# Kernel optimization log

Hardware: AMD Instinct MI355X
Metric: run time of the kernel (lower is better)

The kernel has to match this reference:

```python
import jax, jax.numpy as jnp
import numpy as np

B, C, V = 1024, 512, 256  # batch, num_conjunctions, num_variables


def setup_inputs() -> dict:
    key = jax.random.key(0)
    k1, k2, k3 = jax.random.split(key, 3)
    x0 = jax.random.uniform(k1, (B, V), dtype=jnp.float32)
    # torch init: conj = 1 - 2*rand  -> uniform in (-1, 1)
    conjunctions = 1.0 - 2.0 * jax.random.uniform(k2, (C, 2 * V), dtype=jnp.float32)
    # rw = 10 - 20*rand -> uniform in (-10, 10)
    rule_weights = 10.0 - 20.0 * jax.random.uniform(k3, (C,), dtype=jnp.float32)
    return {"x0": x0, "conjunctions": conjunctions, "rule_weights": rule_weights}


def reference(x0, conjunctions, rule_weights):
    mu = jax.nn.sigmoid(conjunctions)            # (C, 2V)
    x = jnp.concatenate((x0, 1.0 - x0), axis=1)  # (B, 2V)
    # fuzzy-AND: broadcast mul-add then min over literal axis
    x_pot = mu[None, :, :] * x[:, None, :] + (1.0 - mu)[None, :, :]  # (B, C, 2V)
    fit = jnp.min(x_pot, axis=-1)                # (B, C)
    return 5.0 + jnp.sum(rule_weights * fit, axis=-1)  # (B,)
```

## Files before the change

### kernel.cpp

```cpp
#include <hip/hip_runtime.h>


#define B_    1024
#define C_    512
#define V_    256
#define TWOV  512

#define CPW    64
#define NCHUNK (C_ / CPW)
#define BPB    16
#define NBG    (B_ / BPB)
#define WAVES  8
#define VPW    32
#define HVP    8

__global__ __launch_bounds__(256) void k_prep(const float* __restrict__ conj,
                                              float2* __restrict__ muT2,
                                              float* __restrict__ out) {
    const int c = blockIdx.x;
    const int v = threadIdx.x;
    if (c < 4) out[c * 256 + v] = 5.0f;
    float z1 = conj[(size_t)c * TWOV + v];
    float z2 = conj[(size_t)c * TWOV + V_ + v];
    float m1 = 1.0f / (1.0f + __expf(-z1));
    float m2 = 1.0f / (1.0f + __expf(-z2));
    muT2[(size_t)(v >> 1) * (2 * C_) + c * 2 + (v & 1)] = make_float2(m1, m2);
}

__global__ __launch_bounds__(512, 4) void k_main(const float* __restrict__ x0,
                                                 const float4* __restrict__ muT4,
                                                 const float* __restrict__ rw,
                                                 float* __restrict__ out) {
    const int tid   = threadIdx.x;
    const int lane  = tid & 63;
    const int wave  = tid >> 6;
    const int chunk = blockIdx.y;
    const int c     = chunk * CPW + lane;
    const int bg    = blockIdx.x;
    const int v0    = wave * VPW;

    __shared__ float4 xs[BPB * V_ / 4];
    __shared__ float  red[BPB * WAVES * 64];

    {
        const float4* xg = reinterpret_cast<const float4*>(x0 + (size_t)bg * BPB * V_);
        xs[tid]       = xg[tid];
        xs[tid + 512] = xg[tid + 512];
    }

    const float4* mup = muT4 + (size_t)(v0 >> 1) * C_ + c;

    float m[BPB];
#pragma unroll
    for (int i = 0; i < BPB; ++i) m[i] = 0.0f;

    __syncthreads();

#pragma unroll
    for (int h = 0; h < 2; ++h) {
        float4 mr[HVP];
#pragma unroll
        for (int p = 0; p < HVP; ++p)
            mr[p] = mup[(size_t)(h * HVP + p) * C_];
#pragma unroll
        for (int p = 0; p < HVP; ++p)
            asm volatile("" : "+v"(mr[p].x), "+v"(mr[p].y), "+v"(mr[p].z), "+v"(mr[p].w));

#pragma unroll
        for (int bi = 0; bi < BPB; ++bi) {
            const int xb = bi * (V_ / 4) + (v0 >> 2) + h * 4;
            float4 xa = xs[xb + 0];
            float4 xc = xs[xb + 1];
            float4 xd = xs[xb + 2];
            float4 xe = xs[xb + 3];
            float mm = m[bi];
#define STEP(P, XA, XB) \
            mm = fmaxf(mm, fmaxf(__builtin_fmaf(-mr[P].x, (XA), mr[P].x), mr[P].y * (XA))); \
            mm = fmaxf(mm, fmaxf(__builtin_fmaf(-mr[P].z, (XB), mr[P].z), mr[P].w * (XB)));
            STEP(0, xa.x, xa.y)  STEP(1, xa.z, xa.w)
            STEP(2, xc.x, xc.y)  STEP(3, xc.z, xc.w)
            STEP(4, xd.x, xd.y)  STEP(5, xd.z, xd.w)
            STEP(6, xe.x, xe.y)  STEP(7, xe.z, xe.w)
#undef STEP
            m[bi] = mm;
        }
    }

#pragma unroll
    for (int bi = 0; bi < BPB; ++bi)
        red[bi * (WAVES * 64) + tid] = m[bi];
    __syncthreads();

    const float rwc = rw[c];
    float m0 = red[wave * (WAVES * 64) + lane];
    float m1 = red[(wave + 8) * (WAVES * 64) + lane];
#pragma unroll
    for (int k = 1; k < WAVES; ++k) {
        m0 = fmaxf(m0, red[wave * (WAVES * 64) + k * 64 + lane]);
        m1 = fmaxf(m1, red[(wave + 8) * (WAVES * 64) + k * 64 + lane]);
    }
    float s0 = rwc * (1.0f - m0);
    float s1 = rwc * (1.0f - m1);
#pragma unroll
    for (int d = 1; d < 64; d <<= 1) {
        s0 += __shfl_xor(s0, d, 64);
        s1 += __shfl_xor(s1, d, 64);
    }
    if (lane == 0) {
        atomicAdd(&out[bg * BPB + wave], s0);
        atomicAdd(&out[bg * BPB + wave + 8], s1);
    }
}

__global__ __launch_bounds__(256) void k_naive(const float* __restrict__ x0,
                                               const float* __restrict__ conj,
                                               const float* __restrict__ rw,
                                               float* __restrict__ out) {
    int b = blockIdx.x;
    int t = threadIdx.x;
    __shared__ float red[256];
    float acc = 0.0f;
    for (int c = t; c < C_; c += 256) {
        float m = 0.0f;
        for (int v = 0; v < V_; ++v) {
            float mu1 = 1.0f / (1.0f + expf(-conj[(size_t)c * TWOV + v]));
            float mu2 = 1.0f / (1.0f + expf(-conj[(size_t)c * TWOV + V_ + v]));
            float x = x0[(size_t)b * V_ + v];
            m = fmaxf(m, fmaxf(mu1 * (1.0f - x), mu2 * x));
        }
        acc += rw[c] * (1.0f - m);
    }
    red[t] = acc;
    __syncthreads();
    for (int s = 128; s > 0; s >>= 1) {
        if (t < s) red[t] += red[t + s];
        __syncthreads();
    }
    if (t == 0) out[b] = 5.0f + red[0];
}

extern "C" void kernel_launch(void* const* d_in, const int* in_sizes, int n_in,
                              void* d_out, int out_size, void* d_ws, size_t ws_size,
                              hipStream_t stream) {
    const float* x0   = (const float*)d_in[0];
    const float* conj = (const float*)d_in[1];
    const float* rw   = (const float*)d_in[2];
    float* out = (float*)d_out;

    const size_t mu_floats = (size_t)(V_ / 2) * C_ * 4;
    const size_t need = mu_floats * sizeof(float);

    if (ws_size < need) {
        k_naive<<<B_, 256, 0, stream>>>(x0, conj, rw, out);
        return;
    }

    float4* muT4 = (float4*)d_ws;

    k_prep<<<C_, 256, 0, stream>>>(conj, (float2*)muT4, out);
    dim3 grid(NBG, NCHUNK);
    k_main<<<grid, 512, 0, stream>>>(x0, muT4, rw, out);
}
```

Before: 24.89 us.

## Restructure main kernel tiling with register double-buffered global loads instead of LDS

```diff
diff --git a/kernel.cpp b/kernel.cpp
--- a/kernel.cpp
+++ b/kernel.cpp
@@ -6,13 +6,10 @@
 #define V_    256
 #define TWOV  512
 
-#define CPW    64
-#define NCHUNK (C_ / CPW)
-#define BPB    16
+#define BPB    8
 #define NBG    (B_ / BPB)
+#define NCH    4
 #define WAVES  8
-#define VPW    32
-#define HVP    8
 
 __global__ __launch_bounds__(256) void k_prep(const float* __restrict__ conj,
                                               float2* __restrict__ muT2,
@@ -31,84 +28,129 @@
                                                  const float4* __restrict__ muT4,
                                                  const float* __restrict__ rw,
                                                  float* __restrict__ out) {
-    const int tid   = threadIdx.x;
-    const int lane  = tid & 63;
-    const int wave  = tid >> 6;
-    const int chunk = blockIdx.y;
-    const int c     = chunk * CPW + lane;
-    const int bg    = blockIdx.x;
-    const int v0    = wave * VPW;
-
-    __shared__ float4 xs[BPB * V_ / 4];
-    __shared__ float  red[BPB * WAVES * 64];
-
-    {
-        const float4* xg = reinterpret_cast<const float4*>(x0 + (size_t)bg * BPB * V_);
-        xs[tid]       = xg[tid];
-        xs[tid + 512] = xg[tid + 512];
-    }
-
-    const float4* mup = muT4 + (size_t)(v0 >> 1) * C_ + c;
+    const int tid    = threadIdx.x;
+    const int lane   = tid & 63;
+    const int wave_u = __builtin_amdgcn_readfirstlane(tid >> 6);
+    const int t      = wave_u & 1;
+    const int s      = wave_u >> 1;
+    const int bg     = blockIdx.x;
+    const int chunk  = blockIdx.y;
+    const int c      = chunk * 128 + t * 64 + lane;
+    const int v0     = s * 64;
+
+    const float* xb = x0 + (size_t)bg * BPB * V_ + v0;
+
+    const float4* mu1p = muT4 + (size_t)(v0 >> 1) * C_ + c;
+    const float4* mu2p = mu1p + C_;
+
+    const float rwc = rw[c];
 
     float m[BPB];
 #pragma unroll
     for (int i = 0; i < BPB; ++i) m[i] = 0.0f;
 
-    __syncthreads();
-
-#pragma unroll
-    for (int h = 0; h < 2; ++h) {
-        float4 mr[HVP];
-#pragma unroll
-        for (int p = 0; p < HVP; ++p)
-            mr[p] = mup[(size_t)(h * HVP + p) * C_];
-#pragma unroll
-        for (int p = 0; p < HVP; ++p)
-            asm volatile("" : "+v"(mr[p].x), "+v"(mr[p].y), "+v"(mr[p].z), "+v"(mr[p].w));
-
-#pragma unroll
-        for (int bi = 0; bi < BPB; ++bi) {
-            const int xb = bi * (V_ / 4) + (v0 >> 2) + h * 4;
-            float4 xa = xs[xb + 0];
-            float4 xc = xs[xb + 1];
-            float4 xd = xs[xb + 2];
-            float4 xe = xs[xb + 3];
-            float mm = m[bi];
-#define STEP(P, XA, XB) \
-            mm = fmaxf(mm, fmaxf(__builtin_fmaf(-mr[P].x, (XA), mr[P].x), mr[P].y * (XA))); \
-            mm = fmaxf(mm, fmaxf(__builtin_fmaf(-mr[P].z, (XB), mr[P].z), mr[P].w * (XB)));
-            STEP(0, xa.x, xa.y)  STEP(1, xa.z, xa.w)
-            STEP(2, xc.x, xc.y)  STEP(3, xc.z, xc.w)
-            STEP(4, xd.x, xd.y)  STEP(5, xd.z, xd.w)
-            STEP(6, xe.x, xe.y)  STEP(7, xe.z, xe.w)
-#undef STEP
-            m[bi] = mm;
-        }
-    }
-
+    float4 XA0, XA1, XA2, XA3, XA4, XA5, XA6, XA7;
+    float4 XB0, XB1, XB2, XB3, XB4, XB5, XB6, XB7;
+    float4 ma0, mb0, ma1, mb1;
+
+#define XL(X, q) do { \
+    X##0 = *reinterpret_cast<const float4*>(xb + 0 * V_ + 4 * (q)); \
+    X##1 = *reinterpret_cast<const float4*>(xb + 1 * V_ + 4 * (q)); \
+    X##2 = *reinterpret_cast<const float4*>(xb + 2 * V_ + 4 * (q)); \
+    X##3 = *reinterpret_cast<const float4*>(xb + 3 * V_ + 4 * (q)); \
+    X##4 = *reinterpret_cast<const float4*>(xb + 4 * V_ + 4 * (q)); \
+    X##5 = *reinterpret_cast<const float4*>(xb + 5 * V_ + 4 * (q)); \
+    X##6 = *reinterpret_cast<const float4*>(xb + 6 * V_ + 4 * (q)); \
+    X##7 = *reinterpret_cast<const float4*>(xb + 7 * V_ + 4 * (q)); \
+} while (0)
+
+#define MUL_NEXT(MA, MB) do { \
+    MA = mu1p[0]; MB = mu2p[0]; mu1p += 2 * C_; mu2p += 2 * C_; \
+} while (0)
+
+#define PINM(MA, MB) \
+    asm volatile("" : "+v"(MA.x), "+v"(MA.y), "+v"(MA.z), "+v"(MA.w), \
+                      "+v"(MB.x), "+v"(MB.y), "+v"(MB.z), "+v"(MB.w))
+
+#define CB(XV, MA, MB, bi) do { \
+    float mm = m[bi]; \
+    mm = fmaxf(fmaxf(__builtin_fmaf(-(MA).x, (XV).x, (MA).x), (MA).y * (XV).x), mm); \
+    mm = fmaxf(fmaxf(__builtin_fmaf(-(MA).z, (XV).y, (MA).z), (MA).w * (XV).y), mm); \
+    mm = fmaxf(fmaxf(__builtin_fmaf(-(MB).x, (XV).z, (MB).x), (MB).y * (XV).z), mm); \
+    mm = fmaxf(fmaxf(__builtin_fmaf(-(MB).z, (XV).w, (MB).z), (MB).w * (XV).w), mm); \
+    m[bi] = mm; } while (0)
+
+#define COMPUTE(X, MA, MB) do { \
+    CB(X##0, MA, MB, 0); CB(X##1, MA, MB, 1); \
+    CB(X##2, MA, MB, 2); CB(X##3, MA, MB, 3); \
+    CB(X##4, MA, MB, 4); CB(X##5, MA, MB, 5); \
+    CB(X##6, MA, MB, 6); CB(X##7, MA, MB, 7); } while (0)
+
+    XL(XA, 0);
+    MUL_NEXT(ma0, mb0);
+
+#define QSTEP(q, XC, XN, MAC, MBC, MAN, MBN) do { \
+    XL(XN, (q) + 1);               \
+    MUL_NEXT(MAN, MBN);            \
+    PINM(MAC, MBC);                \
+    COMPUTE(XC, MAC, MBC); } while (0)
+
+    QSTEP( 0, XA, XB, ma0, mb0, ma1, mb1);
+    QSTEP( 1, XB, XA, ma1, mb1, ma0, mb0);
+    QSTEP( 2, XA, XB, ma0, mb0, ma1, mb1);
+    QSTEP( 3, XB, XA, ma1, mb1, ma0, mb0);
+    QSTEP( 4, XA, XB, ma0, mb0, ma1, mb1);
+    QSTEP( 5, XB, XA, ma1, mb1, ma0, mb0);
+    QSTEP( 6, XA, XB, ma0, mb0, ma1, mb1);
+    QSTEP( 7, XB, XA, ma1, mb1, ma0, mb0);
+    QSTEP( 8, XA, XB, ma0, mb0, ma1, mb1);
+    QSTEP( 9, XB, XA, ma1, mb1, ma0, mb0);
+    QSTEP(10, XA, XB, ma0, mb0, ma1, mb1);
+    QSTEP(11, XB, XA, ma1, mb1, ma0, mb0);
+    QSTEP(12, XA, XB, ma0, mb0, ma1, mb1);
+    QSTEP(13, XB, XA, ma1, mb1, ma0, mb0);
+    QSTEP(14, XA, XB, ma0, mb0, ma1, mb1);
+    PINM(ma1, mb1);
+    COMPUTE(XB, ma1, mb1);
+
+#undef QSTEP
+#undef COMPUTE
+#undef CB
+#undef PINM
+#undef MUL_NEXT
+#undef XL
+
+    __shared__ float red[4 * 128 * 9];
+    const int ci = t * 64 + lane;
 #pragma unroll
     for (int bi = 0; bi < BPB; ++bi)
-        red[bi * (WAVES * 64) + tid] = m[bi];
+        red[(s * 128 + ci) * 9 + bi] = m[bi];
     __syncthreads();
 
-    const float rwc = rw[c];
-    float m0 = red[wave * (WAVES * 64) + lane];
-    float m1 = red[(wave + 8) * (WAVES * 64) + lane];
-#pragma unroll
-    for (int k = 1; k < WAVES; ++k) {
-        m0 = fmaxf(m0, red[wave * (WAVES * 64) + k * 64 + lane]);
-        m1 = fmaxf(m1, red[(wave + 8) * (WAVES * 64) + k * 64 + lane]);
-    }
-    float s0 = rwc * (1.0f - m0);
-    float s1 = rwc * (1.0f - m1);
-#pragma unroll
-    for (int d = 1; d < 64; d <<= 1) {
-        s0 += __shfl_xor(s0, d, 64);
-        s1 += __shfl_xor(s1, d, 64);
-    }
-    if (lane == 0) {
-        atomicAdd(&out[bg * BPB + wave], s0);
-        atomicAdd(&out[bg * BPB + wave + 8], s1);
+    if (wave_u < 2) {
+        float con0, con1, con2, con3, con4, con5, con6, con7;
+#define FIN(bi, CON) do { \
+        float mm = red[(0 * 128 + ci) * 9 + bi]; \
+        mm = fmaxf(mm, red[(1 * 128 + ci) * 9 + bi]); \
+        mm = fmaxf(mm, red[(2 * 128 + ci) * 9 + bi]); \
+        mm = fmaxf(mm, red[(3 * 128 + ci) * 9 + bi]); \
+        float v = rwc * (1.0f - mm); \
+        v += __shfl_xor(v, 1, 64);  v += __shfl_xor(v, 2, 64); \
+        v += __shfl_xor(v, 4, 64);  v += __shfl_xor(v, 8, 64); \
+        v += __shfl_xor(v, 16, 64); v += __shfl_xor(v, 32, 64); \
+        CON = v; } while (0)
+        FIN(0, con0); FIN(1, con1); FIN(2, con2); FIN(3, con3);
+        FIN(4, con4); FIN(5, con5); FIN(6, con6); FIN(7, con7);
+#undef FIN
+        float t0 = (lane & 1) ? con1 : con0;
+        float t1 = (lane & 1) ? con3 : con2;
+        float t2 = (lane & 1) ? con5 : con4;
+        float t3 = (lane & 1) ? con7 : con6;
+        float u0 = (lane & 2) ? t1 : t0;
+        float u1 = (lane & 2) ? t3 : t2;
+        float sel = (lane & 4) ? u1 : u0;
+        if (lane < 8)
+            atomicAdd(&out[bg * BPB + lane], sel);
     }
 }
 
@@ -158,6 +200,6 @@
     float4* muT4 = (float4*)d_ws;
 
     k_prep<<<C_, 256, 0, stream>>>(conj, (float2*)muT4, out);
-    dim3 grid(NBG, NCHUNK);
+    dim3 grid(NBG, NCH);
     k_main<<<grid, 512, 0, stream>>>(x0, muT4, rw, out);
 }
```

Result: faster. 22.02 us (-11.5%).

## Retile main kernel into 8x4 register blocks with LDS-staged x and mu

Applied to the files above, without the earlier changes.

```diff
diff --git a/kernel.cpp b/kernel.cpp
--- a/kernel.cpp
+++ b/kernel.cpp
@@ -4,111 +4,157 @@
 #define B_    1024
 #define C_    512
 #define V_    256
-#define TWOV  512
-
-#define CPW    64
-#define NCHUNK (C_ / CPW)
-#define BPB    16
-#define NBG    (B_ / BPB)
-#define WAVES  8
-#define VPW    32
-#define HVP    8
+
+#define BT    64
+#define CT    32
+#define VC    128
 
 __global__ __launch_bounds__(256) void k_prep(const float* __restrict__ conj,
-                                              float2* __restrict__ muT2,
+                                              float* __restrict__ muP,
                                               float* __restrict__ out) {
     const int c = blockIdx.x;
     const int v = threadIdx.x;
     if (c < 4) out[c * 256 + v] = 5.0f;
-    float z1 = conj[(size_t)c * TWOV + v];
-    float z2 = conj[(size_t)c * TWOV + V_ + v];
+    float z1 = conj[(size_t)c * 512 + v];
+    float z2 = conj[(size_t)c * 512 + 256 + v];
     float m1 = 1.0f / (1.0f + __expf(-z1));
     float m2 = 1.0f / (1.0f + __expf(-z2));
-    muT2[(size_t)(v >> 1) * (2 * C_) + c * 2 + (v & 1)] = make_float2(m1, m2);
-}
-
-__global__ __launch_bounds__(512, 4) void k_main(const float* __restrict__ x0,
-                                                 const float4* __restrict__ muT4,
+    size_t base = (size_t)v * 1024 + (size_t)(c >> 2) * 8 + (c & 3);
+    muP[base]     = m1;
+    muP[base + 4] = m2;
+}
+
+__global__ __launch_bounds__(512, 2) void k_main(const float* __restrict__ x0,
+                                                 const float* __restrict__ muP,
                                                  const float* __restrict__ rw,
                                                  float* __restrict__ out) {
-    const int tid   = threadIdx.x;
-    const int lane  = tid & 63;
-    const int wave  = tid >> 6;
-    const int chunk = blockIdx.y;
-    const int c     = chunk * CPW + lane;
-    const int bg    = blockIdx.x;
-    const int v0    = wave * VPW;
-
-    __shared__ float4 xs[BPB * V_ / 4];
-    __shared__ float  red[BPB * WAVES * 64];
-
-    {
-        const float4* xg = reinterpret_cast<const float4*>(x0 + (size_t)bg * BPB * V_);
-        xs[tid]       = xg[tid];
-        xs[tid + 512] = xg[tid + 512];
-    }
-
-    const float4* mup = muT4 + (size_t)(v0 >> 1) * C_ + c;
-
-    float m[BPB];
-#pragma unroll
-    for (int i = 0; i < BPB; ++i) m[i] = 0.0f;
-
-    __syncthreads();
-
-#pragma unroll
-    for (int h = 0; h < 2; ++h) {
-        float4 mr[HVP];
-#pragma unroll
-        for (int p = 0; p < HVP; ++p)
-            mr[p] = mup[(size_t)(h * HVP + p) * C_];
-#pragma unroll
-        for (int p = 0; p < HVP; ++p)
-            asm volatile("" : "+v"(mr[p].x), "+v"(mr[p].y), "+v"(mr[p].z), "+v"(mr[p].w));
-
-#pragma unroll
-        for (int bi = 0; bi < BPB; ++bi) {
-            const int xb = bi * (V_ / 4) + (v0 >> 2) + h * 4;
-            float4 xa = xs[xb + 0];
-            float4 xc = xs[xb + 1];
-            float4 xd = xs[xb + 2];
-            float4 xe = xs[xb + 3];
-            float mm = m[bi];
-#define STEP(P, XA, XB) \
-            mm = fmaxf(mm, fmaxf(__builtin_fmaf(-mr[P].x, (XA), mr[P].x), mr[P].y * (XA))); \
-            mm = fmaxf(mm, fmaxf(__builtin_fmaf(-mr[P].z, (XB), mr[P].z), mr[P].w * (XB)));
-            STEP(0, xa.x, xa.y)  STEP(1, xa.z, xa.w)
-            STEP(2, xc.x, xc.y)  STEP(3, xc.z, xc.w)
-            STEP(4, xd.x, xd.y)  STEP(5, xd.z, xd.w)
-            STEP(6, xe.x, xe.y)  STEP(7, xe.z, xe.w)
-#undef STEP
-            m[bi] = mm;
-        }
-    }
-
-#pragma unroll
-    for (int bi = 0; bi < BPB; ++bi)
-        red[bi * (WAVES * 64) + tid] = m[bi];
-    __syncthreads();
-
-    const float rwc = rw[c];
-    float m0 = red[wave * (WAVES * 64) + lane];
-    float m1 = red[(wave + 8) * (WAVES * 64) + lane];
-#pragma unroll
-    for (int k = 1; k < WAVES; ++k) {
-        m0 = fmaxf(m0, red[wave * (WAVES * 64) + k * 64 + lane]);
-        m1 = fmaxf(m1, red[(wave + 8) * (WAVES * 64) + k * 64 + lane]);
-    }
-    float s0 = rwc * (1.0f - m0);
-    float s1 = rwc * (1.0f - m1);
-#pragma unroll
-    for (int d = 1; d < 64; d <<= 1) {
-        s0 += __shfl_xor(s0, d, 64);
-        s1 += __shfl_xor(s1, d, 64);
-    }
-    if (lane == 0) {
-        atomicAdd(&out[bg * BPB + wave], s0);
-        atomicAdd(&out[bg * BPB + wave + 8], s1);
+    __shared__ float lds[16384];
+    const int tid  = threadIdx.x;
+    const int lane = tid & 63;
+    const int w    = tid >> 6;
+    const int ib   = lane & 7;
+    const int jc   = lane >> 3;
+    const int b0   = blockIdx.x * BT;
+    const int c0   = blockIdx.y * CT;
+    const int ib2  = ib * 2;
+
+    float m[8][4];
+#pragma unroll
+    for (int bb = 0; bb < 8; ++bb)
+#pragma unroll
+        for (int cc = 0; cc < 4; ++cc) m[bb][cc] = 0.0f;
+
+    const int xw   = w * 1024;
+    const int mu_b = 8192 + w * 1024 + jc * 8;
+
+#define STAGE(h) do { \
+    _Pragma("unroll") \
+    for (int it = 0; it < 4; ++it) {              \
+        int idx = it * 512 + tid; \
+        int b = idx >> 5, v4 = idx & 31; \
+        float4 xv = *reinterpret_cast<const float4*>( \
+            &x0[(size_t)(b0 + b) * 256 + (h) * 128 + v4 * 4]); \
+        int vb = v4 * 4, gb = b >> 2, bl = b & 3; \
+        lds[(vb+0)*64 + ((gb ^ ((vb+0)&15)) << 2) + bl] = xv.x; \
+        lds[(vb+1)*64 + ((gb ^ ((vb+1)&15)) << 2) + bl] = xv.y; \
+        lds[(vb+2)*64 + ((gb ^ ((vb+2)&15)) << 2) + bl] = xv.z; \
+        lds[(vb+3)*64 + ((gb ^ ((vb+3)&15)) << 2) + bl] = xv.w; \
+    } \
+    _Pragma("unroll") \
+    for (int it = 0; it < 4; ++it) {              \
+        int idx = it * 512 + tid; \
+        int o4 = idx & 15, vl = idx >> 4; \
+        float4 mv = *reinterpret_cast<const float4*>( \
+            &muP[(size_t)((h) * 128 + vl) * 1024 + c0 * 2 + o4 * 4]); \
+        *reinterpret_cast<float4*>(&lds[8192 + vl * 64 + o4 * 4]) = mv; \
+    } } while (0)
+
+#define COMPUTE() do { \
+    _Pragma("unroll") \
+    for (int k = 0; k < 16; ++k) { \
+        int xi = xw + k * 64 + ((ib2 ^ k) << 2); \
+        float4 xa = *reinterpret_cast<const float4*>(&lds[xi]); \
+        float4 xb = *reinterpret_cast<const float4*>(&lds[xi ^ 4]); \
+        float4 av = *reinterpret_cast<const float4*>(&lds[mu_b + k * 64]); \
+        float4 qv = *reinterpret_cast<const float4*>(&lds[mu_b + k * 64 + 4]); \
+        float xs[8] = {xa.x, xa.y, xa.z, xa.w, xb.x, xb.y, xb.z, xb.w}; \
+        float as[4] = {av.x, av.y, av.z, av.w}; \
+        float qs[4] = {qv.x, qv.y, qv.z, qv.w}; \
+        _Pragma("unroll") \
+        for (int bb = 0; bb < 8; ++bb) \
+        _Pragma("unroll") \
+        for (int cc = 0; cc < 4; ++cc) \
+            m[bb][cc] = fmaxf(m[bb][cc], \
+                fmaxf(__builtin_fmaf(-as[cc], xs[bb], as[cc]), qs[cc] * xs[bb])); \
+    } } while (0)
+
+    STAGE(0);
+    __syncthreads();
+    COMPUTE();
+    __syncthreads();
+    STAGE(1);
+    __syncthreads();
+    COMPUTE();
+
+#undef COMPUTE
+#undef STAGE
+
+    __syncthreads();
+#define RED(wi, l, kk) lds[(((wi) * 64 + (l)) * 33) + (kk)]
+    if (w >= 4) {
+#pragma unroll
+        for (int kk = 0; kk < 32; ++kk) RED(w - 4, lane, kk) = m[kk >> 2][kk & 3];
+    }
+    __syncthreads();
+    if (w < 4) {
+#pragma unroll
+        for (int kk = 0; kk < 32; ++kk)
+            m[kk >> 2][kk & 3] = fmaxf(m[kk >> 2][kk & 3], RED(w, lane, kk));
+    }
+    __syncthreads();
+    if (w == 2 || w == 3) {
+#pragma unroll
+        for (int kk = 0; kk < 32; ++kk) RED(w - 2, lane, kk) = m[kk >> 2][kk & 3];
+    }
+    __syncthreads();
+    if (w < 2) {
+#pragma unroll
+        for (int kk = 0; kk < 32; ++kk)
+            m[kk >> 2][kk & 3] = fmaxf(m[kk >> 2][kk & 3], RED(w, lane, kk));
+    }
+    __syncthreads();
+    if (w == 1) {
+#pragma unroll
+        for (int kk = 0; kk < 32; ++kk) RED(0, lane, kk) = m[kk >> 2][kk & 3];
+    }
+    __syncthreads();
+    if (w == 0) {
+#pragma unroll
+        for (int kk = 0; kk < 32; ++kk)
+            m[kk >> 2][kk & 3] = fmaxf(m[kk >> 2][kk & 3], RED(0, lane, kk));
+#undef RED
+        float4 rwv = *reinterpret_cast<const float4*>(&rw[c0 + jc * 4]);
+        float rr[4] = {rwv.x, rwv.y, rwv.z, rwv.w};
+        float val[8];
+#pragma unroll
+        for (int bb = 0; bb < 8; ++bb) {
+            float s = rr[0] * (1.0f - m[bb][0]);
+            s = __builtin_fmaf(rr[1], 1.0f - m[bb][1], s);
+            s = __builtin_fmaf(rr[2], 1.0f - m[bb][2], s);
+            s = __builtin_fmaf(rr[3], 1.0f - m[bb][3], s);
+            val[bb] = s;
+        }
+#pragma unroll
+        for (int bb = 0; bb < 8; ++bb) {
+            val[bb] += __shfl_xor(val[bb], 8, 64);
+            val[bb] += __shfl_xor(val[bb], 16, 64);
+            val[bb] += __shfl_xor(val[bb], 32, 64);
+        }
+        if (jc == 0) {
+#pragma unroll
+            for (int bb = 0; bb < 8; ++bb)
+                atomicAdd(&out[b0 + ib * 8 + bb], val[bb]);
+        }
     }
 }
 
@@ -121,14 +167,14 @@
     __shared__ float red[256];
     float acc = 0.0f;
     for (int c = t; c < C_; c += 256) {
-        float m = 0.0f;
+        float mm = 0.0f;
         for (int v = 0; v < V_; ++v) {
-            float mu1 = 1.0f / (1.0f + expf(-conj[(size_t)c * TWOV + v]));
-            float mu2 = 1.0f / (1.0f + expf(-conj[(size_t)c * TWOV + V_ + v]));
+            float mu1 = 1.0f / (1.0f + expf(-conj[(size_t)c * 512 + v]));
+            float mu2 = 1.0f / (1.0f + expf(-conj[(size_t)c * 512 + 256 + v]));
             float x = x0[(size_t)b * V_ + v];
-            m = fmaxf(m, fmaxf(mu1 * (1.0f - x), mu2 * x));
-        }
-        acc += rw[c] * (1.0f - m);
+            mm = fmaxf(mm, fmaxf(mu1 * (1.0f - x), mu2 * x));
+        }
+        acc += rw[c] * (1.0f - mm);
     }
     red[t] = acc;
     __syncthreads();
@@ -147,7 +193,7 @@
     const float* rw   = (const float*)d_in[2];
     float* out = (float*)d_out;
 
-    const size_t mu_floats = (size_t)(V_ / 2) * C_ * 4;
+    const size_t mu_floats = (size_t)V_ * 1024;
     const size_t need = mu_floats * sizeof(float);
 
     if (ws_size < need) {
@@ -155,9 +201,9 @@
         return;
     }
 
-    float4* muT4 = (float4*)d_ws;
-
-    k_prep<<<C_, 256, 0, stream>>>(conj, (float2*)muT4, out);
-    dim3 grid(NBG, NCHUNK);
-    k_main<<<grid, 512, 0, stream>>>(x0, muT4, rw, out);
-}
+    float* muP = (float*)d_ws;
+
+    k_prep<<<C_, 256, 0, stream>>>(conj, muP, out);
+    dim3 grid(B_ / BT, C_ / CT);
+    k_main<<<grid, 512, 0, stream>>>(x0, muP, rw, out);
+}
```

Result: slower. 29.49 us (+18.5%).
